# Optimization experiments

Measured on AMD Instinct MI355X. Metric: run time of the kernel, lower is better.

## Reference

```python
import jax, jax.numpy as jnp
import numpy as np

HIDDEN = 1024
HEADS = 12
HEAD_DIM = 64
NEG = -1e12


def _rope(x):
    # x: [B, N, H, d], rotate along seq axis (axis 1), interleaved pairs
    B, N, H, d = x.shape
    inv_freq = 1.0 / (10000.0 ** (jnp.arange(0, d, 2, dtype=jnp.float32) / d))  # [d/2]
    pos = jnp.arange(N, dtype=jnp.float32)
    ang = pos[:, None] * inv_freq[None, :]                 # [N, d/2]
    sin = jnp.repeat(jnp.sin(ang), 2, axis=-1)[None, :, None, :]  # [1,N,1,d]
    cos = jnp.repeat(jnp.cos(ang), 2, axis=-1)[None, :, None, :]
    even = x[..., ::2]
    odd = x[..., 1::2]
    rot = jnp.stack([-odd, even], axis=-1).reshape(B, N, H, d)
    return x * cos + rot * sin


def setup_inputs() -> dict:
    key = jax.random.key(0)
    k1, k2, k3, k4 = jax.random.split(key, 4)
    hidden_states = jax.random.normal(k1, (16, 512, HIDDEN), dtype=jnp.float32)
    attention_weights = jax.random.randint(k2, (16, 512), 0, 2, dtype=jnp.int32)
    W = jax.random.normal(k3, (HIDDEN, HEADS * HEAD_DIM * 2), dtype=jnp.float32) * 0.02
    b = jax.random.normal(k4, (HEADS * HEAD_DIM * 2,), dtype=jnp.float32) * 0.02
    return {"hidden_states": hidden_states, "attention_weights": attention_weights, "W": W, "b": b}


def reference(hidden_states, attention_weights, W, b):
    B, N, _ = hidden_states.shape
    proj = hidden_states @ W + b                            # [B,N,H*2*d]
    proj = proj.reshape(B, N, HEADS, 2, HEAD_DIM)
    q, k = proj[..., 0, :], proj[..., 1, :]                 # [B,N,H,d]
    q = _rope(q)
    k = _rope(k)
    q = q / (HEAD_DIM ** 0.5)
    scores = jnp.einsum('bnhd,bmhd->bhnm', q, k)            # [B,H,N,N]
    # mask padded keys (key dim only, matching the torch repeat pattern)
    key_mask = (attention_weights == 0)[:, None, None, :]   # [B,1,1,N]
    scores = jnp.where(key_mask, NEG, scores)
    # mask diagonal
    diag = jnp.eye(N, dtype=bool)[None, None, :, :]
    scores = jnp.where(diag, NEG, scores)
    return jax.nn.sigmoid(scores)
```

## Files before the change

kernel.cpp:

```cpp
#include <hip/hip_runtime.h>

#define HEADS 12
#define HIDDEN 1024
#define NOUT 1536
#define SEQ 512

typedef __bf16 bf16x8 __attribute__((ext_vector_type(8)));
typedef float f32x4 __attribute__((ext_vector_type(4)));

__device__ __forceinline__ void gload_lds16(const void* g, void* l) {
  __builtin_amdgcn_global_load_lds(
      (const __attribute__((address_space(1))) unsigned int*)g,
      (__attribute__((address_space(3))) unsigned int*)l, 16, 0, 0);
}

__device__ __forceinline__ unsigned short f2bf(float f) {
  union { float f; unsigned u; } x;
  x.f = f;
  unsigned r = x.u + 0x7fffu + ((x.u >> 16) & 1u);
  return (unsigned short)(r >> 16);
}

__device__ __forceinline__ int swz8(int b, int per) {
  return (b & 7) * per + (b >> 3);
}

__global__ __launch_bounds__(256) void k_prep(const float* __restrict__ hidden,
                                              unsigned short* __restrict__ hidA,
                                              const float* __restrict__ W,
                                              unsigned short* __restrict__ Wt,
                                              float2* __restrict__ trig) {
  __shared__ unsigned short t[32][33];
  const int bid = blockIdx.x;
  const int tid = threadIdx.x;
  if (bid < 8192) {
    int i = bid * 256 + tid;
    float4 v = ((const float4*)hidden)[i];
    ushort4 o;
    o.x = f2bf(v.x); o.y = f2bf(v.y); o.z = f2bf(v.z); o.w = f2bf(v.w);
    ((ushort4*)hidA)[i] = o;
  } else if (bid < 8192 + 1536) {
    int tt = bid - 8192;
    int n0 = (tt % 48) * 32;
    int k0 = (tt / 48) * 32;
    int tx = tid & 31;
    int ty = tid >> 5;
#pragma unroll
    for (int i = 0; i < 4; ++i) {
      int k = k0 + ty + i * 8;
      t[ty + i * 8][tx] = f2bf(W[(size_t)k * NOUT + n0 + tx]);
    }
    __syncthreads();
#pragma unroll
    for (int i = 0; i < 4; ++i) {
      int n = n0 + ty + i * 8;
      Wt[(size_t)n * HIDDEN + k0 + tx] = t[tx][ty + i * 8];
    }
  } else {
    int i = (bid - 9728) * 256 + tid;
    int pos = i >> 5, j = i & 31;
    float inv = 1.0f / powf(10000.0f, (float)(2 * j) * (1.0f / 64.0f));
    float ang = (float)pos * inv;
    trig[i] = make_float2(cosf(ang), sinf(ang));
  }
}

__global__ __launch_bounds__(256, 3) void k_proj(const unsigned short* __restrict__ A,
                                                 const unsigned short* __restrict__ Bt,
                                                 const float* __restrict__ bias,
                                                 const float2* __restrict__ trig,
                                                 unsigned short* __restrict__ qb,
                                                 unsigned short* __restrict__ kb) {
  __shared__ unsigned short As[3][128 * 32];
  __shared__ unsigned short Bs[3][128 * 32];
  const int lin = swz8(blockIdx.x, 96);
  const int h = lin % 12;
  const int m0 = (lin / 12) * 128;
  const int n0 = h * 128;
  const int tid = threadIdx.x;
  const int wave = tid >> 6, lane = tid & 63;
  const int l15 = lane & 15, l4 = lane >> 4;
  const int wr = wave >> 1, wc = wave & 1;
  const int cchunk = (l4 ^ ((l15 >> 1) & 3)) * 8;

  const int c0 = tid, c1 = 256 + tid;
  const int r0 = c0 >> 2, r1 = c1 >> 2;
  const int s0 = ((c0 & 3) ^ ((r0 >> 1) & 3)) * 8;
  const int s1 = ((c1 & 3) ^ ((r1 >> 1) & 3)) * 8;
  const unsigned short* A0 = A + (size_t)(m0 + r0) * HIDDEN + s0;
  const unsigned short* A1 = A + (size_t)(m0 + r1) * HIDDEN + s1;
  const unsigned short* B0 = Bt + (size_t)(n0 + r0) * HIDDEN + s0;
  const unsigned short* B1 = Bt + (size_t)(n0 + r1) * HIDDEN + s1;

  f32x4 acc[4][4];
#pragma unroll
  for (int a = 0; a < 4; ++a)
#pragma unroll
    for (int b2 = 0; b2 < 4; ++b2) acc[a][b2] = (f32x4){0.f, 0.f, 0.f, 0.f};

#define STAGE(KT, BUF) do {                                   \
    const int kb_ = (KT) * 32;                                \
    gload_lds16(A0 + kb_, &As[BUF][c0 * 8]);                  \
    gload_lds16(A1 + kb_, &As[BUF][c1 * 8]);                  \
    gload_lds16(B0 + kb_, &Bs[BUF][c0 * 8]);                  \
    gload_lds16(B1 + kb_, &Bs[BUF][c1 * 8]);                  \
  } while (0)

#define STEP(KT, CUR, STG, DO_STAGE, VMC) do {                                         \
    if (DO_STAGE) STAGE((KT) + 2, STG);                                                \
    asm volatile("s_waitcnt vmcnt(" #VMC ")" ::: "memory");                            \
    __builtin_amdgcn_s_barrier();                                                      \
    bf16x8 af[4], bv[4];                                                               \
    const unsigned short* Ab_ = &As[CUR][0];                                           \
    const unsigned short* Bb_ = &Bs[CUR][0];                                           \
    _Pragma("unroll") for (int mi = 0; mi < 4; ++mi)                                   \
      af[mi] = *(const bf16x8*)(Ab_ + (wr * 64 + mi * 16 + l15) * 32 + cchunk);        \
    _Pragma("unroll") for (int ni = 0; ni < 4; ++ni)                                   \
      bv[ni] = *(const bf16x8*)(Bb_ + (wc * 64 + ni * 16 + l15) * 32 + cchunk);        \
    __builtin_amdgcn_s_setprio(1);                                                     \
    _Pragma("unroll") for (int mi = 0; mi < 4; ++mi)                                   \
      _Pragma("unroll") for (int ni = 0; ni < 4; ++ni)                                 \
        acc[mi][ni] = __builtin_amdgcn_mfma_f32_16x16x32_bf16(af[mi], bv[ni],          \
                                                              acc[mi][ni], 0, 0, 0);   \
    __builtin_amdgcn_s_setprio(0);                                                     \
    asm volatile("s_waitcnt lgkmcnt(0)" ::: "memory");                                 \
    __builtin_amdgcn_s_barrier();                                                      \
  } while (0)

  STAGE(0, 0);
  STAGE(1, 1);
  for (int t = 0; t < 30; t += 3) {
    STEP(t, 0, 2, true, 8);
    STEP(t + 1, 1, 0, true, 8);
    STEP(t + 2, 2, 1, true, 8);
  }
  STEP(30, 0, 0, false, 4);
  STEP(31, 1, 0, false, 0);
#undef STEP
#undef STAGE

#pragma unroll
  for (int ni = 0; ni < 4; ++ni) {
    const int c = wc * 64 + ni * 16 + l15;
    const int qk = c >> 6;
    const int d = c & 63;
    const int j = d >> 1;
    const int odd = d & 1;
    const float bias_v = bias[n0 + c];
    unsigned short* dst = qk ? kb : qb;
    const float scale = qk ? 1.0f : 0.125f;
#pragma unroll
    for (int mi = 0; mi < 4; ++mi) {
#pragma unroll
      for (int jj = 0; jj < 4; ++jj) {
        const int row = wr * 64 + mi * 16 + l4 * 4 + jj;
        const int m = m0 + row;
        const int bb = m >> 9, pos = m & 511;
        float v = acc[mi][ni][jj] + bias_v;
        float p = __shfl_xor(v, 1);
        float2 cs = trig[pos * 32 + j];
        float o = odd ? (v * cs.x + p * cs.y) : (v * cs.x - p * cs.y);
        o *= scale;
        dst[(((size_t)bb * HEADS + h) * SEQ + pos) * 64 + d] = f2bf(o);
      }
    }
  }
}

__global__ __launch_bounds__(256) void k_scores(const unsigned short* __restrict__ qb,
                                                const unsigned short* __restrict__ kb,
                                                const int* __restrict__ aw,
                                                float* __restrict__ out) {
  __shared__ unsigned short Qs[128 * 64];
  __shared__ unsigned short Ks[2][128 * 64];
  const int lin = swz8(blockIdx.x, 96);
  const int bh = lin >> 2;
  const int b = bh / HEADS;
  const int q0 = (lin & 3) * 128;
  const int tid = threadIdx.x;
  const int wave = tid >> 6, lane = tid & 63;
  const int l15 = lane & 15, l4 = lane >> 4;
  const int wr = wave >> 1, wc = wave & 1;

  const unsigned short* qsrc = qb + (size_t)bh * SEQ * 64 + (size_t)q0 * 64;
  const unsigned short* ksrc = kb + (size_t)bh * SEQ * 64;

#pragma unroll
  for (int i = 0; i < 4; ++i) {
    int chunk = i * 256 + tid;
    gload_lds16(qsrc + chunk * 8, Qs + chunk * 8);
    gload_lds16(ksrc + chunk * 8, &Ks[0][chunk * 8]);
  }
  asm volatile("s_waitcnt vmcnt(0)" ::: "memory");
  __syncthreads();

  for (int tk = 0; tk < 4; ++tk) {
    const int cur = tk & 1;
    const int k0 = tk * 128;

    if (tk < 3) {
      const unsigned short* nsrc = ksrc + (size_t)(k0 + 128) * 64;
#pragma unroll
      for (int i = 0; i < 4; ++i) {
        int chunk = i * 256 + tid;
        gload_lds16(nsrc + chunk * 8, &Ks[cur ^ 1][chunk * 8]);
      }
    }

    f32x4 acc[4][4];
#pragma unroll
    for (int a = 0; a < 4; ++a)
#pragma unroll
      for (int b2 = 0; b2 < 4; ++b2) acc[a][b2] = (f32x4){0.f, 0.f, 0.f, 0.f};

#pragma unroll
    for (int kk = 0; kk < 2; ++kk) {
      bf16x8 qf[4], kf[4];
#pragma unroll
      for (int mi = 0; mi < 4; ++mi)
        qf[mi] = *(const bf16x8*)(Qs + (wr * 64 + mi * 16 + l15) * 64 + kk * 32 + l4 * 8);
#pragma unroll
      for (int ni = 0; ni < 4; ++ni)
        kf[ni] = *(const bf16x8*)(&Ks[cur][0] + (wc * 64 + ni * 16 + l15) * 64 + kk * 32 + l4 * 8);
#pragma unroll
      for (int mi = 0; mi < 4; ++mi)
#pragma unroll
        for (int ni = 0; ni < 4; ++ni)
          acc[mi][ni] = __builtin_amdgcn_mfma_f32_16x16x32_bf16(qf[mi], kf[ni], acc[mi][ni], 0, 0, 0);
    }

#pragma unroll
    for (int ni = 0; ni < 4; ++ni) {
      const int c = wc * 64 + ni * 16 + l15;
      const int key = k0 + c;
      const int awv = aw[b * SEQ + key];
#pragma unroll
      for (int mi = 0; mi < 4; ++mi) {
#pragma unroll
        for (int jj = 0; jj < 4; ++jj) {
          const int row = wr * 64 + mi * 16 + l4 * 4 + jj;
          const int nq = q0 + row;
          float s = acc[mi][ni][jj];
          float o = (awv == 0 || nq == key) ? 0.0f : 1.0f / (1.0f + __expf(-s));
          out[((size_t)bh * SEQ + nq) * SEQ + key] = o;
        }
      }
    }

    __syncthreads();
  }
}

extern "C" void kernel_launch(void* const* d_in, const int* in_sizes, int n_in,
                              void* d_out, int out_size, void* d_ws, size_t ws_size,
                              hipStream_t stream) {
  const float* hidden = (const float*)d_in[0];
  const int* aw = (const int*)d_in[1];
  const float* W = (const float*)d_in[2];
  const float* bias = (const float*)d_in[3];
  float* out = (float*)d_out;

  char* ws = (char*)d_ws;
  unsigned short* hidA = (unsigned short*)ws;
  unsigned short* Wt = (unsigned short*)(ws + 16777216);
  unsigned short* qb = (unsigned short*)(ws + 19922944);
  unsigned short* kb = (unsigned short*)(ws + 32505856);
  float2* trig = (float2*)(ws + 45088768);

  k_prep<<<9792, 256, 0, stream>>>(hidden, hidA, W, Wt, trig);
  k_proj<<<768, 256, 0, stream>>>(hidA, Wt, bias, trig, qb, kb);
  k_scores<<<768, 256, 0, stream>>>(qb, kb, aw, out);
}
```

Measured before the change: 105.4 us.

## Prefetch two K tiles ahead with counted waits and pair output stores into float2

The scores kernel now loads Q and the first two K tiles up front. It replaces the full vmcnt(0) waits and __syncthreads with partial vmcnt counts plus raw s_barrier, so more global-to-LDS loads stay in flight across tiles. The epilogue swaps sigmoid results between adjacent lanes with a shuffle, so each lane writes two 8-byte float2 stores instead of four scalar 4-byte stores. The goal is less load latency exposure and wider output writes on this output-bound kernel. The risk is that the hand-counted vmcnt values can be wrong, because the stores also increment vmcnt, which could cause races or over-waiting.

```diff
diff --git a/kernel.cpp b/kernel.cpp
--- a/kernel.cpp
+++ b/kernel.cpp
@@ -181,6 +181,7 @@
   const int wave = tid >> 6, lane = tid & 63;
   const int l15 = lane & 15, l4 = lane >> 4;
   const int wr = wave >> 1, wc = wave & 1;
+  const int oddlane = lane & 1;
 
   const unsigned short* qsrc = qb + (size_t)bh * SEQ * 64 + (size_t)q0 * 64;
   const unsigned short* ksrc = kb + (size_t)bh * SEQ * 64;
@@ -189,16 +190,25 @@
   for (int i = 0; i < 4; ++i) {
     int chunk = i * 256 + tid;
     gload_lds16(qsrc + chunk * 8, Qs + chunk * 8);
+  }
+#pragma unroll
+  for (int i = 0; i < 4; ++i) {
+    int chunk = i * 256 + tid;
     gload_lds16(ksrc + chunk * 8, &Ks[0][chunk * 8]);
   }
-  asm volatile("s_waitcnt vmcnt(0)" ::: "memory");
-  __syncthreads();
+#pragma unroll
+  for (int i = 0; i < 4; ++i) {
+    int chunk = i * 256 + tid;
+    gload_lds16(ksrc + (size_t)128 * 64 + chunk * 8, &Ks[1][chunk * 8]);
+  }
+  asm volatile("s_waitcnt vmcnt(4)" ::: "memory");
+  __builtin_amdgcn_s_barrier();
 
   for (int tk = 0; tk < 4; ++tk) {
     const int cur = tk & 1;
     const int k0 = tk * 128;
 
-    if (tk < 3) {
+    if (tk == 1 || tk == 2) {
       const unsigned short* nsrc = ksrc + (size_t)(k0 + 128) * 64;
 #pragma unroll
       for (int i = 0; i < 4; ++i) {
@@ -206,6 +216,13 @@
         gload_lds16(nsrc + chunk * 8, &Ks[cur ^ 1][chunk * 8]);
       }
     }
+    if (tk == 1 || tk == 2) {
+      asm volatile("s_waitcnt vmcnt(36)" ::: "memory");
+      __builtin_amdgcn_s_barrier();
+    } else if (tk == 3) {
+      asm volatile("s_waitcnt vmcnt(32)" ::: "memory");
+      __builtin_amdgcn_s_barrier();
+    }
 
     f32x4 acc[4][4];
 #pragma unroll
@@ -233,21 +250,33 @@
     for (int ni = 0; ni < 4; ++ni) {
       const int c = wc * 64 + ni * 16 + l15;
       const int key = k0 + c;
+      const int keybase = key & ~1;
       const int awv = aw[b * SEQ + key];
 #pragma unroll
       for (int mi = 0; mi < 4; ++mi) {
+        float o[4], p[4];
 #pragma unroll
         for (int jj = 0; jj < 4; ++jj) {
           const int row = wr * 64 + mi * 16 + l4 * 4 + jj;
           const int nq = q0 + row;
           float s = acc[mi][ni][jj];
-          float o = (awv == 0 || nq == key) ? 0.0f : 1.0f / (1.0f + __expf(-s));
-          out[((size_t)bh * SEQ + nq) * SEQ + key] = o;
+          o[jj] = (awv == 0 || nq == key) ? 0.0f : 1.0f / (1.0f + __expf(-s));
         }
+#pragma unroll
+        for (int jj = 0; jj < 4; ++jj) p[jj] = __shfl_xor(o[jj], 1);
+        const int rbase = q0 + wr * 64 + mi * 16 + l4 * 4 + (oddlane ? 2 : 0);
+        float2 s0, s1;
+        s0.x = oddlane ? p[2] : o[0];
+        s0.y = oddlane ? o[2] : p[0];
+        s1.x = oddlane ? p[3] : o[1];
+        s1.y = oddlane ? o[3] : p[1];
+        float* obase = out + (size_t)bh * SEQ * SEQ + keybase;
+        *(float2*)(obase + (size_t)rbase * SEQ) = s0;
+        *(float2*)(obase + (size_t)(rbase + 1) * SEQ) = s1;
       }
     }
 
-    __syncthreads();
+    if (tk < 3) __builtin_amdgcn_s_barrier();
   }
 }
 
```

Measured after the change: 107.9 us. 1.02x slower.
